# Kernel optimization log

Hardware: AMD Instinct MI355X
Metric: run time of the kernel (lower is better)

Reference implementation:

```python
import jax, jax.numpy as jnp
import numpy as np

N_KNOTS = 4096
N_QUERIES = 33554432  # 32M query points (~128MB fp32)


def _pchip_derivatives(x, y):
    # Vectorized version of the original O(n) Python loop.
    dx = x[1:] - x[:-1]                      # [n-1]
    slopes = (y[1:] - y[:-1]) / dx           # [n-1]
    s0, s1 = slopes[:-1], slopes[1:]         # [n-2] neighbouring slopes
    dx0, dx1 = dx[:-1], dx[1:]
    cond = (s0 * s1) > 0                     # same-sign slopes -> harmonic mean
    w1 = 2.0 * dx1 + dx0
    w2 = dx1 + 2.0 * dx0
    # guard divisions so the where() is NaN-free
    s0s = jnp.where(cond, s0, 1.0)
    s1s = jnp.where(cond, s1, 1.0)
    d_mid = jnp.where(cond, (w1 + w2) / (w1 / s0s + w2 / s1s), 0.0)
    return jnp.concatenate([slopes[:1], d_mid, slopes[-1:]])  # [n]


def setup_inputs() -> dict:
    key = jax.random.key(0)
    k_y, k_t = jax.random.split(key)
    x = jnp.arange(N_KNOTS, dtype=jnp.float32)               # sorted knots
    y = jax.random.normal(k_y, (N_KNOTS,), dtype=jnp.float32)
    t = jax.random.uniform(k_t, (N_QUERIES,), dtype=jnp.float32) * (N_KNOTS - 1)
    return {"x": x, "y": y, "t": t}


def reference(x, y, t):
    d = _pchip_derivatives(x, y)
    n_seg = x.shape[0] - 1  # self.n
    # searchsorted (left, like torch default) then clamp to valid segment
    idx = jnp.clip(jnp.searchsorted(x, t) - 1, 0, n_seg - 1)
    x0 = x[idx]
    x1 = x[idx + 1]
    y0 = y[idx]
    y1 = y[idx + 1]
    d0 = d[idx]
    d1 = d[idx + 1]
    dx_seg = x1 - x0
    tn = (t - x0) / dx_seg
    t2 = tn * tn
    t3 = t2 * tn
    h00 = 2.0 * t3 - 3.0 * t2 + 1.0
    h10 = t3 - 2.0 * t2 + tn
    h01 = -2.0 * t3 + 3.0 * t2
    h11 = t3 - t2
    return h00 * y0 + h10 * dx_seg * d0 + h01 * y1 + h11 * dx_seg * d1
```

## Files before the change

### kernel.cpp

```cpp
#include <hip/hip_runtime.h>

#define N_KNOTS 4096
#define N_SEG (N_KNOTS - 1)
#define BLOCK 256

__device__ __forceinline__ float pchip_eval(float tq, const float* ys, const float* ds) {
    int idx = (int)tq;
    idx = min(max(idx, 0), N_SEG - 1);
    float tn = tq - (float)idx;
    float y0 = ys[idx];
    float y1 = ys[idx + 1];
    float d0 = ds[idx];
    float d1 = ds[idx + 1];
    float t2 = tn * tn;
    float t3 = t2 * tn;
    float h00 = 2.0f * t3 - 3.0f * t2 + 1.0f;
    float h10 = t3 - 2.0f * t2 + tn;
    float h01 = 3.0f * t2 - 2.0f * t3;
    float h11 = t3 - t2;
    return h00 * y0 + h10 * d0 + h01 * y1 + h11 * d1;
}

__global__ __launch_bounds__(BLOCK) void pchip_kernel(
    const float* __restrict__ y,
    const float* __restrict__ t,
    float* __restrict__ out,
    int n_queries)
{
    __shared__ float ys[N_KNOTS];
    __shared__ float ds[N_KNOTS];

    for (int i = threadIdx.x; i < N_KNOTS; i += BLOCK)
        ys[i] = y[i];
    __syncthreads();

    for (int i = threadIdx.x; i < N_KNOTS; i += BLOCK) {
        float dval;
        if (i == 0) {
            dval = ys[1] - ys[0];
        } else if (i == N_KNOTS - 1) {
            dval = ys[N_KNOTS - 1] - ys[N_KNOTS - 2];
        } else {
            float s0 = ys[i] - ys[i - 1];
            float s1 = ys[i + 1] - ys[i];
            dval = (s0 * s1 > 0.0f) ? (6.0f / (3.0f / s0 + 3.0f / s1)) : 0.0f;
        }
        ds[i] = dval;
    }
    __syncthreads();

    const int n4 = n_queries >> 2;
    const float4* __restrict__ t4 = (const float4*)t;
    float4* __restrict__ o4 = (float4*)out;
    const int stride = gridDim.x * blockDim.x;

    for (int i = blockIdx.x * blockDim.x + threadIdx.x; i < n4; i += stride) {
        float4 tv = t4[i];
        float4 r;
        r.x = pchip_eval(tv.x, ys, ds);
        r.y = pchip_eval(tv.y, ys, ds);
        r.z = pchip_eval(tv.z, ys, ds);
        r.w = pchip_eval(tv.w, ys, ds);
        o4[i] = r;
    }

    const int tail_start = n4 << 2;
    for (int i = tail_start + blockIdx.x * blockDim.x + threadIdx.x;
         i < n_queries; i += stride) {
        out[i] = pchip_eval(t[i], ys, ds);
    }
}

extern "C" void kernel_launch(void* const* d_in, const int* in_sizes, int n_in,
                              void* d_out, int out_size, void* d_ws, size_t ws_size,
                              hipStream_t stream) {
    const float* y = (const float*)d_in[1];
    const float* t = (const float*)d_in[2];
    float* out = (float*)d_out;
    const int n_queries = in_sizes[2];

    const int blocks = 2048;
    pchip_kernel<<<blocks, BLOCK, 0, stream>>>(y, t, out, n_queries);
}
```

Measured before the change: 55.95 us.

## Precompute per-segment cubic coefficients in LDS and evaluate with Horner FMAs

Each segment's Hermite basis is turned into cubic polynomial coefficients (a, b, c, d), stored as a float4 in shared memory. Each query then does one 16-byte LDS read plus three FMAs instead of four scalar LDS reads and the full basis arithmetic. Output stores become nontemporal, and the launch moves to 512 blocks of 1024 threads. Each block now reads y directly from global memory to build the table, and the Horner form may change rounding slightly.

```diff
diff --git a/kernel.cpp b/kernel.cpp
--- a/kernel.cpp
+++ b/kernel.cpp
@@ -2,72 +2,86 @@
 
 #define N_KNOTS 4096
 #define N_SEG (N_KNOTS - 1)
-#define BLOCK 256
+#define BLOCK 1024
 
-__device__ __forceinline__ float pchip_eval(float tq, const float* ys, const float* ds) {
-    int idx = (int)tq;
-    idx = min(max(idx, 0), N_SEG - 1);
-    float tn = tq - (float)idx;
-    float y0 = ys[idx];
-    float y1 = ys[idx + 1];
-    float d0 = ds[idx];
-    float d1 = ds[idx + 1];
-    float t2 = tn * tn;
-    float t3 = t2 * tn;
-    float h00 = 2.0f * t3 - 3.0f * t2 + 1.0f;
-    float h10 = t3 - 2.0f * t2 + tn;
-    float h01 = 3.0f * t2 - 2.0f * t3;
-    float h11 = t3 - t2;
-    return h00 * y0 + h10 * d0 + h01 * y1 + h11 * d1;
-}
+typedef float f32x4 __attribute__((ext_vector_type(4)));
 
-__global__ __launch_bounds__(BLOCK) void pchip_kernel(
+__global__ __launch_bounds__(BLOCK, 8) void pchip_kernel(
     const float* __restrict__ y,
     const float* __restrict__ t,
     float* __restrict__ out,
     int n_queries)
 {
-    __shared__ float ys[N_KNOTS];
-    __shared__ float ds[N_KNOTS];
+    __shared__ float4 coef[N_SEG];
 
-    for (int i = threadIdx.x; i < N_KNOTS; i += BLOCK)
-        ys[i] = y[i];
-    __syncthreads();
-
-    for (int i = threadIdx.x; i < N_KNOTS; i += BLOCK) {
-        float dval;
+    for (int i = threadIdx.x; i < N_SEG; i += BLOCK) {
+        float y0 = y[i];
+        float y1 = y[i + 1];
+        float s0 = y1 - y0;
+        float d0, d1;
         if (i == 0) {
-            dval = ys[1] - ys[0];
-        } else if (i == N_KNOTS - 1) {
-            dval = ys[N_KNOTS - 1] - ys[N_KNOTS - 2];
+            d0 = s0;
         } else {
-            float s0 = ys[i] - ys[i - 1];
-            float s1 = ys[i + 1] - ys[i];
-            dval = (s0 * s1 > 0.0f) ? (6.0f / (3.0f / s0 + 3.0f / s1)) : 0.0f;
+            float sm = y0 - y[i - 1];
+            d0 = (sm * s0 > 0.0f) ? (2.0f * sm * s0) / (sm + s0) : 0.0f;
         }
-        ds[i] = dval;
+        if (i == N_SEG - 1) {
+            d1 = s0;
+        } else {
+            float sp = y[i + 2] - y1;
+            d1 = (s0 * sp > 0.0f) ? (2.0f * s0 * sp) / (s0 + sp) : 0.0f;
+        }
+        float a = y0;
+        float b = d0;
+        float c = 3.0f * (y1 - y0) - 2.0f * d0 - d1;
+        float dd = 2.0f * (y0 - y1) + d0 + d1;
+        coef[i] = make_float4(a, b, c, dd);
     }
     __syncthreads();
 
     const int n4 = n_queries >> 2;
     const float4* __restrict__ t4 = (const float4*)t;
-    float4* __restrict__ o4 = (float4*)out;
+    f32x4* __restrict__ o4 = (f32x4*)out;
     const int stride = gridDim.x * blockDim.x;
 
     for (int i = blockIdx.x * blockDim.x + threadIdx.x; i < n4; i += stride) {
         float4 tv = t4[i];
-        float4 r;
-        r.x = pchip_eval(tv.x, ys, ds);
-        r.y = pchip_eval(tv.y, ys, ds);
-        r.z = pchip_eval(tv.z, ys, ds);
-        r.w = pchip_eval(tv.w, ys, ds);
-        o4[i] = r;
+        f32x4 r;
+        {
+            int idx = min(max((int)tv.x, 0), N_SEG - 1);
+            float tn = tv.x - (float)idx;
+            float4 cf = coef[idx];
+            r.x = fmaf(fmaf(fmaf(cf.w, tn, cf.z), tn, cf.y), tn, cf.x);
+        }
+        {
+            int idx = min(max((int)tv.y, 0), N_SEG - 1);
+            float tn = tv.y - (float)idx;
+            float4 cf = coef[idx];
+            r.y = fmaf(fmaf(fmaf(cf.w, tn, cf.z), tn, cf.y), tn, cf.x);
+        }
+        {
+            int idx = min(max((int)tv.z, 0), N_SEG - 1);
+            float tn = tv.z - (float)idx;
+            float4 cf = coef[idx];
+            r.z = fmaf(fmaf(fmaf(cf.w, tn, cf.z), tn, cf.y), tn, cf.x);
+        }
+        {
+            int idx = min(max((int)tv.w, 0), N_SEG - 1);
+            float tn = tv.w - (float)idx;
+            float4 cf = coef[idx];
+            r.w = fmaf(fmaf(fmaf(cf.w, tn, cf.z), tn, cf.y), tn, cf.x);
+        }
+        __builtin_nontemporal_store(r, &o4[i]);
     }
 
     const int tail_start = n4 << 2;
     for (int i = tail_start + blockIdx.x * blockDim.x + threadIdx.x;
          i < n_queries; i += stride) {
-        out[i] = pchip_eval(t[i], ys, ds);
+        float tq = t[i];
+        int idx = min(max((int)tq, 0), N_SEG - 1);
+        float tn = tq - (float)idx;
+        float4 cf = coef[idx];
+        out[i] = fmaf(fmaf(fmaf(cf.w, tn, cf.z), tn, cf.y), tn, cf.x);
     }
 }
 
@@ -79,6 +93,6 @@
     float* out = (float*)d_out;
     const int n_queries = in_sizes[2];
 
-    const int blocks = 2048;
+    const int blocks = 512;
     pchip_kernel<<<blocks, BLOCK, 0, stream>>>(y, t, out, n_queries);
 }
```

After: 47.61 us. 1.18x faster.
